# Kernel tuning notes

Hardware: AMD Instinct MI355X
Metric: run time of the kernel (lower is better)

The kernel has to match this reference:

```python
import jax, jax.numpy as jnp
import numpy as np

B, C, H, W = 8, 16, 256, 256
HID = 32

def setup_inputs() -> dict:
    key = jax.random.key(0)
    ks = jax.random.split(key, 6)
    swin_logits = jax.random.normal(ks[0], (B, C, H, W), dtype=jnp.float32)
    gru_logits = jax.random.normal(ks[1], (B, C, H, W), dtype=jnp.float32)
    # per-class gate params (stacked across classes); torch Linear default-ish scale
    W1 = jax.random.normal(ks[2], (C, HID, 2), dtype=jnp.float32) * (1.0 / np.sqrt(2.0))
    b1 = jax.random.normal(ks[3], (C, HID), dtype=jnp.float32) * 0.1
    W2 = jax.random.normal(ks[4], (C, 2, HID), dtype=jnp.float32) * (1.0 / np.sqrt(HID))
    b2 = jax.random.normal(ks[5], (C, 2), dtype=jnp.float32) * 0.1
    # expert_preferences initialized exactly as in the torch module
    pref = np.zeros((C, 2), dtype=np.float32)
    for i in range(C):
        w_hls = 0.3 + 0.4 * (i / max(1, C - 1))
        pref[i] = [w_hls, 1.0 - w_hls]
    expert_preferences = jnp.asarray(pref)
    return {"swin_logits": swin_logits, "gru_logits": gru_logits,
            "W1": W1, "b1": b1, "W2": W2, "b2": b2,
            "expert_preferences": expert_preferences}

def reference(swin_logits, gru_logits, W1, b1, W2, b2, expert_preferences):
    b, c, h, w = swin_logits.shape
    # class-dim softmax over logits
    swin_probs = jax.nn.softmax(swin_logits, axis=1)
    gru_probs = jax.nn.softmax(gru_logits, axis=1)
    # (B,C,H,W) -> (N,C), N = B*H*W
    sp = swin_probs.transpose(0, 2, 3, 1).reshape(-1, c)
    gp = gru_probs.transpose(0, 2, 3, 1).reshape(-1, c)
    gate_in = jnp.stack([sp, gp], axis=-1)  # (N, C, 2)
    # batched per-class gate MLP (Dropout is identity in eval mode)
    hid = jax.nn.relu(jnp.einsum('nci,chi->nch', gate_in, W1) + b1)  # (N,C,HID)
    dynamic_weights = jax.nn.softmax(jnp.einsum('nch,coh->nco', hid, W2) + b2, axis=-1)  # (N,C,2)
    # weighted fusion of expert logits
    sl = swin_logits.transpose(0, 2, 3, 1).reshape(-1, c)
    gl = gru_logits.transpose(0, 2, 3, 1).reshape(-1, c)
    expert_logits = jnp.stack([sl, gl], axis=-1)  # (N,C,2)
    fused_flat = jnp.sum(dynamic_weights * expert_logits, axis=-1)  # (N,C)
    fused_logits = fused_flat.reshape(b, h, w, c).transpose(0, 3, 1, 2)
    return fused_logits, expert_preferences, dynamic_weights
```

## Files before the change

### kernel.cpp

```cpp
#include <hip/hip_runtime.h>

typedef float v2f __attribute__((ext_vector_type(2)));

#define Bc   8
#define Cc   16
#define HWc  65536
#define HIDc 32
#define Npix (Bc * HWc)
#define FUSED_ELEMS (Bc * Cc * HWc)
#define PREF_ELEMS  (Cc * 2)
#define TPB  256
#define WSTRIDE 65
#define PACKED_BYTES (Cc * WSTRIDE * 8)

__global__ void gate_prep(const float* __restrict__ W1, const float* __restrict__ b1,
                          const float* __restrict__ W2, const float* __restrict__ b2,
                          v2f* __restrict__ ws)
{
    const int c = blockIdx.x;
    const int j = threadIdx.x;
    v2f* wp = ws + c * WSTRIDE;
    if (j < 16) {
        wp[j]      = (v2f){W1[c*64 + 4*j + 0], W1[c*64 + 4*j + 2]};
        wp[16 + j] = (v2f){W1[c*64 + 4*j + 1], W1[c*64 + 4*j + 3]};
        wp[32 + j] = (v2f){b1[c*32 + 2*j],     b1[c*32 + 2*j + 1]};
        wp[48 + j] = (v2f){W2[c*64 + 2*j]     - W2[c*64 + 32 + 2*j],
                           W2[c*64 + 2*j + 1] - W2[c*64 + 32 + 2*j + 1]};
    } else if (j == 16) {
        wp[64] = (v2f){b2[2*c] - b2[2*c + 1], 0.f};
    }
}

__global__ __launch_bounds__(TPB)
__attribute__((amdgpu_waves_per_eu(6, 6)))
void gate_main_packed(
    const float* __restrict__ swin, const float* __restrict__ gru,
    const v2f* __restrict__ wsw, const float* __restrict__ pref,
    float* __restrict__ out)
{
    const int tid  = threadIdx.x;
    const int n    = blockIdx.x * TPB + tid;
    const int bidx = n >> 16;
    const int hw   = n & (HWc - 1);

    const float* sptr = swin + (size_t)bidx * (Cc * HWc) + hw;
    const float* gptr = gru  + (size_t)bidx * (Cc * HWc) + hw;

    float sl[Cc], gl[Cc];
#pragma unroll
    for (int c = 0; c < Cc; ++c) {
        sl[c] = sptr[c * HWc];
        gl[c] = gptr[c * HWc];
    }

    float ss0 = 0.f, ss1 = 0.f, sg0 = 0.f, sg1 = 0.f;
#pragma unroll
    for (int c = 0; c < Cc; c += 2) {
        ss0 += __expf(sl[c]);     sg0 += __expf(gl[c]);
        ss1 += __expf(sl[c + 1]); sg1 += __expf(gl[c + 1]);
    }
    const float invs = __builtin_amdgcn_rcpf(ss0 + ss1);
    const float invg = __builtin_amdgcn_rcpf(sg0 + sg1);

    float* fop = out + (size_t)bidx * (Cc * HWc) + hw;

    float w0a[Cc];
#pragma unroll
    for (int c = 0; c < Cc; ++c) {
        const float sp = __expf(sl[c]) * invs;
        const float gp = __expf(gl[c]) * invg;
        const v2f spv = {sp, sp};
        const v2f gpv = {gp, gp};

        const v2f* wp = wsw + c * WSTRIDE;

        v2f acc = {0.f, 0.f};
#pragma unroll
        for (int j = 0; j < HIDc / 2; ++j) {
            v2f h = wp[j] * spv + (wp[16 + j] * gpv + wp[32 + j]);
            h = __builtin_elementwise_max(h, (v2f){0.f, 0.f});
            acc = h * wp[48 + j] + acc;
        }
        const float d = acc.x + acc.y + wp[64].x;

        const float t = __expf(-fabsf(d));
        const float r = __builtin_amdgcn_rcpf(1.f + t);
        const float w0 = (d >= 0.f) ? r : 1.f - r;
        const float w1 = 1.f - w0;

        fop[c * HWc] = fmaf(w0, sl[c], w1 * gl[c]);
        w0a[c] = w0;
    }

    float4* dwp = reinterpret_cast<float4*>(
        out + (size_t)FUSED_ELEMS + PREF_ELEMS + (size_t)n * (Cc * 2));
#pragma unroll
    for (int k = 0; k < Cc / 2; ++k) {
        dwp[k] = make_float4(w0a[2*k],     1.f - w0a[2*k],
                             w0a[2*k + 1], 1.f - w0a[2*k + 1]);
    }

    if (blockIdx.x == 0 && tid < PREF_ELEMS) {
        out[(size_t)FUSED_ELEMS + tid] = pref[tid];
    }
}

__global__ __launch_bounds__(TPB, 4) void gate_main_scalar(
    const float* __restrict__ swin, const float* __restrict__ gru,
    const float* __restrict__ W1, const float* __restrict__ b1,
    const float* __restrict__ W2, const float* __restrict__ b2,
    const float* __restrict__ pref, float* __restrict__ out)
{
    __shared__ float2 dwbuf2[TPB * Cc];

    const int tid  = threadIdx.x;
    const int n    = blockIdx.x * TPB + tid;
    const int bidx = n >> 16;
    const int hw   = n & (HWc - 1);

    const float* sptr = swin + (size_t)bidx * (Cc * HWc) + hw;
    const float* gptr = gru  + (size_t)bidx * (Cc * HWc) + hw;

    float sl[Cc], gl[Cc];
#pragma unroll
    for (int c = 0; c < Cc; ++c) { sl[c] = sptr[c * HWc]; gl[c] = gptr[c * HWc]; }

    float ms = sl[0], mg = gl[0];
#pragma unroll
    for (int c = 1; c < Cc; ++c) { ms = fmaxf(ms, sl[c]); mg = fmaxf(mg, gl[c]); }
    float es[Cc], eg[Cc];
    float ss = 0.f, sg = 0.f;
#pragma unroll
    for (int c = 0; c < Cc; ++c) {
        es[c] = __expf(sl[c] - ms);  ss += es[c];
        eg[c] = __expf(gl[c] - mg);  sg += eg[c];
    }
    const float invs = __builtin_amdgcn_rcpf(ss);
    const float invg = __builtin_amdgcn_rcpf(sg);

    float* fop = out + (size_t)bidx * (Cc * HWc) + hw;

#pragma unroll
    for (int c = 0; c < Cc; ++c) {
        const float sp = es[c] * invs;
        const float gp = eg[c] * invg;
        const float* w1c = W1 + c * (HIDc * 2);
        const float* b1c = b1 + c * HIDc;
        const float* w2c = W2 + c * (2 * HIDc);

        float a0 = b2[c * 2 + 0];
        float a1 = b2[c * 2 + 1];
#pragma unroll
        for (int k = 0; k < HIDc; ++k) {
            float h = fmaf(w1c[k * 2 + 0], sp, fmaf(w1c[k * 2 + 1], gp, b1c[k]));
            h = fmaxf(h, 0.f);
            a0 = fmaf(w2c[k], h, a0);
            a1 = fmaf(w2c[HIDc + k], h, a1);
        }
        const float d = a0 - a1;
        const float t = __expf(-fabsf(d));
        const float r = __builtin_amdgcn_rcpf(1.f + t);
        const float w0 = (d >= 0.f) ? r : 1.f - r;
        const float w1 = 1.f - w0;

        fop[c * HWc] = fmaf(w0, sl[c], w1 * gl[c]);
        dwbuf2[tid * Cc + ((c + tid) & (Cc - 1))] = make_float2(w0, w1);
    }

    __syncthreads();

    float2* outv2 = reinterpret_cast<float2*>(
        out + (size_t)FUSED_ELEMS + PREF_ELEMS + (size_t)blockIdx.x * (TPB * Cc * 2));
#pragma unroll
    for (int j = 0; j < Cc; ++j) {
        const int pi = j * TPB + tid;
        const int p  = pi >> 4;
        const int pr = pi & (Cc - 1);
        outv2[pi] = dwbuf2[p * Cc + ((pr + p) & (Cc - 1))];
    }

    if (blockIdx.x == 0 && tid < PREF_ELEMS) {
        out[(size_t)FUSED_ELEMS + tid] = pref[tid];
    }
}

extern "C" void kernel_launch(void* const* d_in, const int* in_sizes, int n_in,
                              void* d_out, int out_size, void* d_ws, size_t ws_size,
                              hipStream_t stream) {
    const float* swin = (const float*)d_in[0];
    const float* gru  = (const float*)d_in[1];
    const float* W1   = (const float*)d_in[2];
    const float* b1   = (const float*)d_in[3];
    const float* W2   = (const float*)d_in[4];
    const float* b2   = (const float*)d_in[5];
    const float* pref = (const float*)d_in[6];
    float* out = (float*)d_out;

    dim3 block(TPB);

    if (ws_size >= (size_t)PACKED_BYTES) {
        v2f* ws = (v2f*)d_ws;
        hipLaunchKernelGGL(gate_prep, dim3(Cc), dim3(64), 0, stream, W1, b1, W2, b2, ws);
        hipLaunchKernelGGL(gate_main_packed, dim3(Npix / TPB), block, 0, stream,
                           swin, gru, ws, pref, out);
    } else {
        hipLaunchKernelGGL(gate_main_scalar, dim3(Npix / TPB), block, 0, stream,
                           swin, gru, W1, b1, W2, b2, pref, out);
    }
}
```

Measured before the change: 197.7 us.

## Split classes across four wave groups per pixel with LDS softmax reduction

```diff
diff --git a/kernel.cpp b/kernel.cpp
--- a/kernel.cpp
+++ b/kernel.cpp
@@ -10,6 +10,8 @@
 #define FUSED_ELEMS (Bc * Cc * HWc)
 #define PREF_ELEMS  (Cc * 2)
 #define TPB  256
+#define PXB  64
+#define CPG  4
 #define WSTRIDE 65
 #define PACKED_BYTES (Cc * WSTRIDE * 8)
 
@@ -32,47 +34,61 @@
 }
 
 __global__ __launch_bounds__(TPB)
-__attribute__((amdgpu_waves_per_eu(6, 6)))
-void gate_main_packed(
+__attribute__((amdgpu_waves_per_eu(6, 8)))
+void gate_main_split(
     const float* __restrict__ swin, const float* __restrict__ gru,
     const v2f* __restrict__ wsw, const float* __restrict__ pref,
     float* __restrict__ out)
 {
-    const int tid  = threadIdx.x;
-    const int n    = blockIdx.x * TPB + tid;
+    __shared__ float part[2][4][PXB];
+    __shared__ float wlds[PXB][17];
+
+    const int tid = threadIdx.x;
+    const int px  = tid & 63;
+    const int cg  = tid >> 6;
+
+    const int n    = blockIdx.x * PXB + px;
     const int bidx = n >> 16;
     const int hw   = n & (HWc - 1);
-
-    const float* sptr = swin + (size_t)bidx * (Cc * HWc) + hw;
-    const float* gptr = gru  + (size_t)bidx * (Cc * HWc) + hw;
-
-    float sl[Cc], gl[Cc];
-#pragma unroll
-    for (int c = 0; c < Cc; ++c) {
-        sl[c] = sptr[c * HWc];
-        gl[c] = gptr[c * HWc];
-    }
-
-    float ss0 = 0.f, ss1 = 0.f, sg0 = 0.f, sg1 = 0.f;
-#pragma unroll
-    for (int c = 0; c < Cc; c += 2) {
-        ss0 += __expf(sl[c]);     sg0 += __expf(gl[c]);
-        ss1 += __expf(sl[c + 1]); sg1 += __expf(gl[c + 1]);
-    }
-    const float invs = __builtin_amdgcn_rcpf(ss0 + ss1);
-    const float invg = __builtin_amdgcn_rcpf(sg0 + sg1);
-
-    float* fop = out + (size_t)bidx * (Cc * HWc) + hw;
-
-    float w0a[Cc];
-#pragma unroll
-    for (int c = 0; c < Cc; ++c) {
-        const float sp = __expf(sl[c]) * invs;
-        const float gp = __expf(gl[c]) * invg;
+    const size_t ibase = (size_t)bidx * (Cc * HWc) + hw;
+
+    const float* sptr = swin + ibase;
+    const float* gptr = gru  + ibase;
+
+    float sl[CPG], gl[CPG];
+#pragma unroll
+    for (int i = 0; i < CPG; ++i) {
+        const int c = cg * CPG + i;
+        sl[i] = sptr[c * HWc];
+        gl[i] = gptr[c * HWc];
+    }
+
+    float ss = 0.f, sg = 0.f;
+#pragma unroll
+    for (int i = 0; i < CPG; ++i) {
+        ss += __expf(sl[i]);
+        sg += __expf(gl[i]);
+    }
+    part[0][cg][px] = ss;
+    part[1][cg][px] = sg;
+    __syncthreads();
+
+    const float invs = __builtin_amdgcn_rcpf(
+        part[0][0][px] + part[0][1][px] + part[0][2][px] + part[0][3][px]);
+    const float invg = __builtin_amdgcn_rcpf(
+        part[1][0][px] + part[1][1][px] + part[1][2][px] + part[1][3][px]);
+
+    float* fop = out + ibase;
+
+#pragma unroll
+    for (int i = 0; i < CPG; ++i) {
+        const int c = __builtin_amdgcn_readfirstlane(cg * CPG + i);
+        const v2f* wp = wsw + c * WSTRIDE;
+
+        const float sp = __expf(sl[i]) * invs;
+        const float gp = __expf(gl[i]) * invg;
         const v2f spv = {sp, sp};
         const v2f gpv = {gp, gp};
-
-        const v2f* wp = wsw + c * WSTRIDE;
 
         v2f acc = {0.f, 0.f};
 #pragma unroll
@@ -88,17 +104,23 @@
         const float w0 = (d >= 0.f) ? r : 1.f - r;
         const float w1 = 1.f - w0;
 
-        fop[c * HWc] = fmaf(w0, sl[c], w1 * gl[c]);
-        w0a[c] = w0;
-    }
-
+        fop[c * HWc] = fmaf(w0, sl[i], w1 * gl[i]);
+        wlds[px][c] = w0;
+    }
+    __syncthreads();
+
+    const int px2 = tid >> 2;
+    const int q   = tid & 3;
+    const int n2  = blockIdx.x * PXB + px2;
     float4* dwp = reinterpret_cast<float4*>(
-        out + (size_t)FUSED_ELEMS + PREF_ELEMS + (size_t)n * (Cc * 2));
-#pragma unroll
-    for (int k = 0; k < Cc / 2; ++k) {
-        dwp[k] = make_float4(w0a[2*k],     1.f - w0a[2*k],
-                             w0a[2*k + 1], 1.f - w0a[2*k + 1]);
-    }
+        out + (size_t)FUSED_ELEMS + PREF_ELEMS + (size_t)n2 * (Cc * 2));
+
+    const float a0 = wlds[px2][2 * q];
+    const float a1 = wlds[px2][2 * q + 1];
+    const float b0 = wlds[px2][2 * q + 8];
+    const float b1 = wlds[px2][2 * q + 9];
+    dwp[q]     = make_float4(a0, 1.f - a0, a1, 1.f - a1);
+    dwp[q + 4] = make_float4(b0, 1.f - b0, b1, 1.f - b1);
 
     if (blockIdx.x == 0 && tid < PREF_ELEMS) {
         out[(size_t)FUSED_ELEMS + tid] = pref[tid];
@@ -201,7 +223,7 @@
     if (ws_size >= (size_t)PACKED_BYTES) {
         v2f* ws = (v2f*)d_ws;
         hipLaunchKernelGGL(gate_prep, dim3(Cc), dim3(64), 0, stream, W1, b1, W2, b2, ws);
-        hipLaunchKernelGGL(gate_main_packed, dim3(Npix / TPB), block, 0, stream,
+        hipLaunchKernelGGL(gate_main_split, dim3(Npix / PXB), block, 0, stream,
                            swin, gru, ws, pref, out);
     } else {
         hipLaunchKernelGGL(gate_main_scalar, dim3(Npix / TPB), block, 0, stream,
```

After: 170.3 us. 13.9% less time.
